# Performance work log

Hardware: AMD Instinct MI355X
Metric: run time of the kernel (lower is better)

The kernel has to match this reference:

```python
import jax, jax.numpy as jnp
import numpy as np

B, S, D = 8, 2048, 768
SCALE = jnp.sqrt(jnp.float32(D))


def setup_inputs() -> dict:
    key = jax.random.key(0)
    ks = jax.random.split(key, 9)
    sd = 1.0 / np.sqrt(D)
    return {
        "x": jax.random.normal(ks[0], (B, S, D), jnp.float32),
        "Wq": jax.random.normal(ks[1], (D, D), jnp.float32) * sd,
        "bq": jax.random.normal(ks[2], (D,), jnp.float32) * sd,
        "Wk": jax.random.normal(ks[3], (D, D), jnp.float32) * sd,
        "bk": jax.random.normal(ks[4], (D,), jnp.float32) * sd,
        "Wv": jax.random.normal(ks[5], (D, D), jnp.float32) * sd,
        "bv": jax.random.normal(ks[6], (D,), jnp.float32) * sd,
        "Wp": jax.random.normal(ks[7], (D, D), jnp.float32) * sd,
        "bp": jax.random.normal(ks[8], (D,), jnp.float32) * sd,
    }


def reference(x, Wq, bq, Wk, bk, Wv, bv, Wp, bp):
    # Linear layers: y = x @ W^T + b (torch nn.Linear convention)
    Q = jnp.einsum("bsd,ed->bse", x, Wq) + bq
    K = jnp.einsum("bsd,ed->bse", x, Wk) + bk
    V = jnp.einsum("bsd,ed->bse", x, Wv) + bv
    # Full attention matrix (no head split in original module)
    alpha = jnp.einsum("bqd,bkd->bqk", Q, K) / SCALE  # [B,S,S]
    alpha = jax.nn.softmax(alpha, axis=-1)
    # dropout is identity in eval mode
    out = jnp.einsum("bqk,bkd->bqd", alpha, V)
    out = jnp.einsum("bsd,ed->bse", out, Wp) + bp
    return out
```

## Files before the change

kernel.cpp:

```cpp
#include <hip/hip_runtime.h>
#include <stdint.h>


typedef __attribute__((ext_vector_type(8))) short short8;
typedef __attribute__((ext_vector_type(4))) float f32x4;

typedef const __attribute__((address_space(1))) void gvoid_t;
typedef __attribute__((address_space(3))) void lvoid_t;

__device__ __forceinline__ float b2f(unsigned short u) {
  union { unsigned int u; float f; } v;
  v.u = ((unsigned int)u) << 16;
  return v.f;
}
__device__ __forceinline__ unsigned short f2b(float f) {
  union { float f; unsigned int u; } v; v.f = f;
  unsigned int u = v.u;
  return (unsigned short)((u + 0x7fffu + ((u >> 16) & 1u)) >> 16);
}

struct Cvt9 {
  const void* s[9];
  unsigned short* d[9];
  long long n8[9];
  long long total8;
};

__global__ __launch_bounds__(256) void convert_inputs(Cvt9 C) {
  long long g = (long long)blockIdx.x * 256 + threadIdx.x;
  if (g >= C.total8) return;
  int s = 0;
  long long off = g;
  while (off >= C.n8[s]) { off -= C.n8[s]; ++s; }
  const float* sf = (const float*)C.s[s] + off * 8;
  unsigned short* dp = C.d[s] + off * 8;
  float4 a = ((const float4*)sf)[0];
  float4 b = ((const float4*)sf)[1];
  uint4 o;
  o.x = (unsigned int)f2b(a.x) | ((unsigned int)f2b(a.y) << 16);
  o.y = (unsigned int)f2b(a.z) | ((unsigned int)f2b(a.w) << 16);
  o.z = (unsigned int)f2b(b.x) | ((unsigned int)f2b(b.y) << 16);
  o.w = (unsigned int)f2b(b.z) | ((unsigned int)f2b(b.w) << 16);
  *(uint4*)dp = o;
}

__device__ __forceinline__ void gemm256(
    const unsigned short* __restrict__ Ag,
    const unsigned short* __restrict__ Bg,
    const int lda, const int ldb, const int NT,
    unsigned short* lds, f32x4 (&acc)[4][4])
{
  const int t    = threadIdx.x;
  const int w    = t >> 6;
  const int lane = t & 63;
  const int lo   = lane & 15;
  const int quad = lane >> 4;
  const int wr   = w >> 1;
  const int wc   = w & 1;
  const int srow = t >> 2;
  const int ssw  = ((t & 3) ^ ((t >> 3) & 3)) << 3;

  const unsigned lbase = (unsigned)(uintptr_t)(void*)lds;
  const unsigned rsw   = (unsigned)((quad ^ ((lo >> 1) & 3)) << 4);
  const unsigned aAr   = lbase + (unsigned)(wr * 64 + lo) * 64 + rsw;
  const unsigned aBr   = lbase + 16384u + (unsigned)(wc * 64 + lo) * 64 + rsw;

#define STG(kt, buf) {                                                              \
  const unsigned short* a0_ = Ag + (size_t)(srow)       * lda + (kt) * 32 + ssw;    \
  const unsigned short* a1_ = Ag + (size_t)(128 + srow) * lda + (kt) * 32 + ssw;    \
  const unsigned short* b0_ = Bg + (size_t)(srow)       * ldb + (kt) * 32 + ssw;    \
  unsigned short* d_ = lds + (buf) * 12288 + t * 8;                                 \
  __builtin_amdgcn_global_load_lds((gvoid_t*)a0_, (lvoid_t*)(d_),        16, 0, 0); \
  __builtin_amdgcn_global_load_lds((gvoid_t*)a1_, (lvoid_t*)(d_ + 4096), 16, 0, 0); \
  __builtin_amdgcn_global_load_lds((gvoid_t*)b0_, (lvoid_t*)(d_ + 8192), 16, 0, 0); }
#define DSR(d, a, IMM) asm volatile("ds_read_b128 %0, %1 offset:" #IMM : "=v"(d) : "v"(a))
#define LGK(n) { asm volatile("s_waitcnt lgkmcnt(" #n ")" ::: "memory"); \
                 __builtin_amdgcn_sched_barrier(0); }
#define GRP(g) { _Pragma("unroll") for (int mi = 0; mi < 4; ++mi)             \
    acc[mi][g] = __builtin_amdgcn_mfma_f32_16x16x32_bf16(                     \
        af[mi], bf[g], acc[mi][g], 0, 0, 0); }

  STG(0, 0);
  __syncthreads();

  for (int kt = 0; kt < NT; ++kt) {
    const int buf = kt & 1;
    if (kt + 1 < NT) STG(kt + 1, buf ^ 1);

    const unsigned bo = (unsigned)(buf * 24576);
    short8 af[4], bf[4];
    const unsigned aA = aAr + bo, aB = aBr + bo;
    DSR(af[0], aA, 0); DSR(af[1], aA, 1024); DSR(af[2], aA, 2048); DSR(af[3], aA, 3072);
    DSR(bf[0], aB, 0); DSR(bf[1], aB, 1024); DSR(bf[2], aB, 2048); DSR(bf[3], aB, 3072);

    __builtin_amdgcn_s_setprio(1);
    LGK(3); GRP(0);
    LGK(2); GRP(1);
    LGK(1); GRP(2);
    LGK(0); GRP(3);
    __builtin_amdgcn_s_setprio(0);

    __syncthreads();
  }
#undef STG
#undef DSR
#undef LGK
#undef GRP
}

template<int MODE>
__device__ __forceinline__ void epi_bf16(
    unsigned short* Ls, f32x4 (&acc)[4][4],
    const unsigned short* bias_n0, const float* rlbase, float scale,
    unsigned short* Cg, int ldc, float* rlout)
{
  const int t = threadIdx.x, w = t >> 6, lane = t & 63;
  const int lo = lane & 15, quad = lane >> 4, wr = w >> 1, wc = w & 1;
#pragma unroll
  for (int h = 0; h < 2; ++h) {
    __syncthreads();
    if ((wr >> 1) == h) {
      float bvv[4];
      if (MODE == 0) {
#pragma unroll
        for (int ni = 0; ni < 4; ++ni) bvv[ni] = b2f(bias_n0[wc * 64 + ni * 16 + lo]);
      }
#pragma unroll
      for (int mi = 0; mi < 4; ++mi) {
        const int r0 = (wr & 1) * 64 + mi * 16 + quad * 4;
        float rv[4];
        if (MODE == 3) {
#pragma unroll
          for (int r = 0; r < 4; ++r) rv[r] = __builtin_amdgcn_rcpf(rlbase[h * 128 + r0 + r]);
        }
#pragma unroll
        for (int ni = 0; ni < 4; ++ni) {
          const int col = wc * 64 + ni * 16 + lo;
#pragma unroll
          for (int r = 0; r < 4; ++r) {
            float v = acc[mi][ni][r];
            if (MODE == 0)      v += bvv[ni];
            else if (MODE == 2) v = __expf(fminf(v * scale, 30.f));
            else if (MODE == 3) v *= rv[r];
            Ls[(r0 + r) * 136 + col] = f2b(v);
          }
        }
      }
    }
    __syncthreads();
#pragma unroll
    for (int j = 0; j < 4; ++j) {
      const int u = j * 512 + t, row = u >> 4, c16 = (u & 15) * 8;
      *(uint4*)(Cg + (size_t)(h * 128 + row) * ldc + c16) = *(const uint4*)(Ls + row * 136 + c16);
    }
    if (MODE == 2) {
      const int row = t >> 2, seg = t & 3;
      const unsigned short* lr = Ls + row * 136 + seg * 32;
      float s = 0.f;
#pragma unroll
      for (int q4 = 0; q4 < 4; ++q4) {
        uint4 v = *(const uint4*)(lr + q4 * 8);
        unsigned int uu[4] = {v.x, v.y, v.z, v.w};
#pragma unroll
        for (int c = 0; c < 4; ++c)
          s += b2f((unsigned short)(uu[c] & 0xffffu)) + b2f((unsigned short)(uu[c] >> 16));
      }
      s += __shfl_xor(s, 1);
      s += __shfl_xor(s, 2);
      if (seg == 0) atomicAdd(rlout + h * 128 + row, s);
    }
  }
}

__global__ __launch_bounds__(512, 4) void qkv_k(
    const unsigned short* __restrict__ xb,
    const unsigned short* __restrict__ Wq, const unsigned short* __restrict__ bq,
    const unsigned short* __restrict__ Wk, const unsigned short* __restrict__ bk,
    const unsigned short* __restrict__ Wv, const unsigned short* __restrict__ bv,
    unsigned short* __restrict__ qb, unsigned short* __restrict__ kb,
    unsigned short* __restrict__ vt)
{
  __shared__ unsigned short smem[24576];
  const int sel = blockIdx.y / 6;
  const int n0  = (blockIdx.y % 6) * 128;
  const int m0  = blockIdx.x * 256;

  const unsigned short* W;
  const unsigned short* bi;
  if (sel == 0)      { W = Wq; bi = bq; }
  else if (sel == 1) { W = Wk; bi = bk; }
  else               { W = Wv; bi = bv; }

  f32x4 acc[4][4] = {};
  gemm256(xb + (size_t)m0 * 768, W + (size_t)n0 * 768, 768, 768, 24, smem, acc);

  if (sel < 2) {
    unsigned short* dst = (sel == 0 ? qb : kb) + (size_t)m0 * 768 + n0;
    epi_bf16<0>(smem, acc, bi + n0, nullptr, 0.f, dst, 768, nullptr);
    return;
  }

  const int t = threadIdx.x, w = t >> 6, lane = t & 63;
  const int lo = lane & 15, quad = lane >> 4, wr = w >> 1, wc = w & 1;
  const int bb2 = m0 >> 11, sin = m0 & 2047;
  unsigned short* Ls = smem;
#pragma unroll
  for (int ec = 0; ec < 2; ++ec) {
    __syncthreads();
    if (wc == ec) {
#pragma unroll
      for (int ni = 0; ni < 4; ++ni) {
        const int el = ni * 16 + lo;
        const float bvv = b2f(bi[n0 + ec * 64 + el]);
#pragma unroll
        for (int mi = 0; mi < 4; ++mi) {
          const int sl = wr * 64 + mi * 16 + quad * 4;
          ushort4 pk;
          pk.x = f2b(acc[mi][ni][0] + bvv);
          pk.y = f2b(acc[mi][ni][1] + bvv);
          pk.z = f2b(acc[mi][ni][2] + bvv);
          pk.w = f2b(acc[mi][ni][3] + bvv);
          *(ushort4*)(Ls + el * 264 + sl) = pk;
        }
      }
    }
    __syncthreads();
    unsigned short* Vb = vt + (size_t)bb2 * 1572864 + (size_t)(n0 + ec * 64) * 2048 + sin;
#pragma unroll
    for (int j = 0; j < 4; ++j) {
      const int u = j * 512 + t, e = u >> 5, s16 = (u & 31) * 8;
      *(uint4*)(Vb + (size_t)e * 2048 + s16) = *(const uint4*)(Ls + e * 264 + s16);
    }
  }
}

__global__ __launch_bounds__(512, 4) void score_k(
    const unsigned short* __restrict__ Q, const unsigned short* __restrict__ Kb,
    unsigned short* __restrict__ E, float* __restrict__ rl, float scale)
{
  __shared__ unsigned short smem[24576];
  const int m0 = blockIdx.x * 256, n0 = blockIdx.y * 128, bz = blockIdx.z;

  f32x4 acc[4][4] = {};
  gemm256(Q + (size_t)bz * 1572864 + (size_t)m0 * 768,
          Kb + (size_t)bz * 1572864 + (size_t)n0 * 768, 768, 768, 24, smem, acc);

  unsigned short* Eg = E + (size_t)bz * 4194304 + (size_t)m0 * 2048 + n0;
  epi_bf16<2>(smem, acc, nullptr, nullptr, scale, Eg, 2048, rl + bz * 2048 + m0);
}

__global__ __launch_bounds__(512, 4) void pv_k(
    const unsigned short* __restrict__ E, const unsigned short* __restrict__ Vt,
    const float* __restrict__ rl, unsigned short* __restrict__ attn)
{
  __shared__ unsigned short smem[24576];
  const int m0 = blockIdx.x * 256, n0 = blockIdx.y * 128, bz = blockIdx.z;

  f32x4 acc[4][4] = {};
  gemm256(E + (size_t)bz * 4194304 + (size_t)m0 * 2048,
          Vt + (size_t)bz * 1572864 + (size_t)n0 * 2048, 2048, 2048, 64, smem, acc);

  const float* rlb = rl + bz * 2048 + m0;
  unsigned short* Cg = attn + (size_t)bz * 1572864 + (size_t)m0 * 768 + n0;
  epi_bf16<3>(smem, acc, nullptr, rlb, 0.f, Cg, 768, nullptr);
}

__global__ __launch_bounds__(512, 4) void out_k(
    const unsigned short* __restrict__ attn,
    const unsigned short* __restrict__ Wp, const unsigned short* __restrict__ bp,
    float* __restrict__ Of)
{
  __shared__ unsigned short smem[24576];
  const int m0 = blockIdx.x * 256, n0 = blockIdx.y * 128;

  f32x4 acc[4][4] = {};
  gemm256(attn + (size_t)m0 * 768, Wp + (size_t)n0 * 768, 768, 768, 24, smem, acc);

  const int t = threadIdx.x, w = t >> 6, lane = t & 63;
  const int lo = lane & 15, quad = lane >> 4, wr = w >> 1, wc = w & 1;
  float* Lf = (float*)smem;
#pragma unroll
  for (int p = 0; p < 4; ++p) {
    __syncthreads();
    if (wr == p) {
#pragma unroll
      for (int mi = 0; mi < 4; ++mi) {
        const int r0 = mi * 16 + quad * 4;
#pragma unroll
        for (int ni = 0; ni < 4; ++ni) {
          const int col = wc * 64 + ni * 16 + lo;
          const float bvv = b2f(bp[n0 + col]);
#pragma unroll
          for (int r = 0; r < 4; ++r)
            Lf[(r0 + r) * 132 + col] = acc[mi][ni][r] + bvv;
        }
      }
    }
    __syncthreads();
#pragma unroll
    for (int j = 0; j < 2; ++j) {
      const int u = j * 512 + t, row = u >> 4, c4 = (u & 15) * 8;
      const float* src = Lf + row * 132 + c4;
      float4 v0 = *(const float4*)(src);
      float4 v1 = *(const float4*)(src + 4);
      float* dst = Of + (size_t)(m0 + p * 64 + row) * 768 + n0 + c4;
      *(float4*)(dst) = v0;
      *(float4*)(dst + 4) = v1;
    }
  }
}

extern "C" void kernel_launch(void* const* d_in, const int* in_sizes, int n_in,
                              void* d_out, int out_size, void* d_ws, size_t ws_size,
                              hipStream_t stream) {
  (void)in_sizes; (void)n_in; (void)out_size; (void)ws_size;

  char* ws = (char*)d_ws;
  float* rl    = (float*)(ws + 4096);
  unsigned short* wcv = (unsigned short*)(ws + ((size_t)1 << 20));
  unsigned short* qb  = (unsigned short*)(ws + ((size_t)8  << 20));
  unsigned short* kb  = (unsigned short*)(ws + ((size_t)32 << 20));
  unsigned short* vt  = (unsigned short*)(ws + ((size_t)56 << 20));
  unsigned short* eb  = (unsigned short*)(ws + ((size_t)80 << 20));
  unsigned short* xb  = eb;
  unsigned short* attn = qb;

  unsigned short* wqb = wcv;
  unsigned short* bqb = wcv + 589824;
  unsigned short* wkb = wcv + 590592;
  unsigned short* bkb = wcv + 1180416;
  unsigned short* wvb = wcv + 1181184;
  unsigned short* bvb = wcv + 1771008;
  unsigned short* wpb = wcv + 1771776;
  unsigned short* bpb = wcv + 2361600;

  const float inv_scale = 0.036084391824351615f;

  Cvt9 cv;
  cv.s[0] = d_in[0]; cv.d[0] = xb;  cv.n8[0] = 12582912 / 8;
  cv.s[1] = d_in[1]; cv.d[1] = wqb; cv.n8[1] = 589824 / 8;
  cv.s[2] = d_in[2]; cv.d[2] = bqb; cv.n8[2] = 768 / 8;
  cv.s[3] = d_in[3]; cv.d[3] = wkb; cv.n8[3] = 589824 / 8;
  cv.s[4] = d_in[4]; cv.d[4] = bkb; cv.n8[4] = 768 / 8;
  cv.s[5] = d_in[5]; cv.d[5] = wvb; cv.n8[5] = 589824 / 8;
  cv.s[6] = d_in[6]; cv.d[6] = bvb; cv.n8[6] = 768 / 8;
  cv.s[7] = d_in[7]; cv.d[7] = wpb; cv.n8[7] = 589824 / 8;
  cv.s[8] = d_in[8]; cv.d[8] = bpb; cv.n8[8] = 768 / 8;
  cv.total8 = (12582912 + 4 * (589824 + 768)) / 8;
  convert_inputs<<<(unsigned)((cv.total8 + 255) / 256), dim3(256), 0, stream>>>(cv);

  hipMemsetAsync(rl, 0, 16384 * sizeof(float), stream);

  qkv_k<<<dim3(64, 18, 1), dim3(512), 0, stream>>>(xb, wqb, bqb, wkb, bkb, wvb, bvb, qb, kb, vt);

  score_k<<<dim3(8, 16, 8), dim3(512), 0, stream>>>(qb, kb, eb, rl, inv_scale);

  pv_k<<<dim3(8, 6, 8), dim3(512), 0, stream>>>(eb, vt, rl, attn);

  out_k<<<dim3(64, 6, 1), dim3(512), 0, stream>>>(attn, wpb, bpb, (float*)d_out);
}
```

Measured before the change: 342.2 us.

## Halve block size and double per-wave M tile in all GEMM kernels

Each GEMM block now runs 4 waves (256 threads) instead of 8. Every wave computes a 128x64 output tile with 8x4 MFMA accumulators, where before it was 64x64. Staging issues six global-to-LDS loads per thread instead of three, and the epilogues are reindexed to match. The goal is more MFMA work per LDS fragment read and fewer waves per block. The cost is doubled accumulator registers, which could cut occupancy or cause spills, and less parallelism for hiding latency.

```diff
diff --git a/kernel.cpp b/kernel.cpp
--- a/kernel.cpp
+++ b/kernel.cpp
@@ -48,11 +48,11 @@
     const unsigned short* __restrict__ Ag,
     const unsigned short* __restrict__ Bg,
     const int lda, const int ldb, const int NT,
-    unsigned short* lds, f32x4 (&acc)[4][4])
+    unsigned short* lds, f32x4 (&acc)[8][4])
 {
   const int t    = threadIdx.x;
+  const int lane = t & 63;
   const int w    = t >> 6;
-  const int lane = t & 63;
   const int lo   = lane & 15;
   const int quad = lane >> 4;
   const int wr   = w >> 1;
@@ -62,21 +62,27 @@
 
   const unsigned lbase = (unsigned)(uintptr_t)(void*)lds;
   const unsigned rsw   = (unsigned)((quad ^ ((lo >> 1) & 3)) << 4);
-  const unsigned aAr   = lbase + (unsigned)(wr * 64 + lo) * 64 + rsw;
+  const unsigned aAr   = lbase + (unsigned)(wr * 128 + lo) * 64 + rsw;
   const unsigned aBr   = lbase + 16384u + (unsigned)(wc * 64 + lo) * 64 + rsw;
 
 #define STG(kt, buf) {                                                              \
   const unsigned short* a0_ = Ag + (size_t)(srow)       * lda + (kt) * 32 + ssw;    \
-  const unsigned short* a1_ = Ag + (size_t)(128 + srow) * lda + (kt) * 32 + ssw;    \
+  const unsigned short* a1_ = Ag + (size_t)(64 + srow)  * lda + (kt) * 32 + ssw;    \
+  const unsigned short* a2_ = Ag + (size_t)(128 + srow) * lda + (kt) * 32 + ssw;    \
+  const unsigned short* a3_ = Ag + (size_t)(192 + srow) * lda + (kt) * 32 + ssw;    \
   const unsigned short* b0_ = Bg + (size_t)(srow)       * ldb + (kt) * 32 + ssw;    \
+  const unsigned short* b1_ = Bg + (size_t)(64 + srow)  * ldb + (kt) * 32 + ssw;    \
   unsigned short* d_ = lds + (buf) * 12288 + t * 8;                                 \
-  __builtin_amdgcn_global_load_lds((gvoid_t*)a0_, (lvoid_t*)(d_),        16, 0, 0); \
-  __builtin_amdgcn_global_load_lds((gvoid_t*)a1_, (lvoid_t*)(d_ + 4096), 16, 0, 0); \
-  __builtin_amdgcn_global_load_lds((gvoid_t*)b0_, (lvoid_t*)(d_ + 8192), 16, 0, 0); }
+  __builtin_amdgcn_global_load_lds((gvoid_t*)a0_, (lvoid_t*)(d_),         16, 0, 0);\
+  __builtin_amdgcn_global_load_lds((gvoid_t*)a1_, (lvoid_t*)(d_ + 2048),  16, 0, 0);\
+  __builtin_amdgcn_global_load_lds((gvoid_t*)a2_, (lvoid_t*)(d_ + 4096),  16, 0, 0);\
+  __builtin_amdgcn_global_load_lds((gvoid_t*)a3_, (lvoid_t*)(d_ + 6144),  16, 0, 0);\
+  __builtin_amdgcn_global_load_lds((gvoid_t*)b0_, (lvoid_t*)(d_ + 8192),  16, 0, 0);\
+  __builtin_amdgcn_global_load_lds((gvoid_t*)b1_, (lvoid_t*)(d_ + 10240), 16, 0, 0); }
 #define DSR(d, a, IMM) asm volatile("ds_read_b128 %0, %1 offset:" #IMM : "=v"(d) : "v"(a))
 #define LGK(n) { asm volatile("s_waitcnt lgkmcnt(" #n ")" ::: "memory"); \
                  __builtin_amdgcn_sched_barrier(0); }
-#define GRP(g) { _Pragma("unroll") for (int mi = 0; mi < 4; ++mi)             \
+#define GRP(g) { _Pragma("unroll") for (int mi = 0; mi < 8; ++mi)             \
     acc[mi][g] = __builtin_amdgcn_mfma_f32_16x16x32_bf16(                     \
         af[mi], bf[g], acc[mi][g], 0, 0, 0); }
 
@@ -88,10 +94,14 @@
     if (kt + 1 < NT) STG(kt + 1, buf ^ 1);
 
     const unsigned bo = (unsigned)(buf * 24576);
-    short8 af[4], bf[4];
+    short8 af[8], bf[4];
     const unsigned aA = aAr + bo, aB = aBr + bo;
-    DSR(af[0], aA, 0); DSR(af[1], aA, 1024); DSR(af[2], aA, 2048); DSR(af[3], aA, 3072);
-    DSR(bf[0], aB, 0); DSR(bf[1], aB, 1024); DSR(bf[2], aB, 2048); DSR(bf[3], aB, 3072);
+    DSR(af[0], aA, 0);    DSR(af[1], aA, 1024);
+    DSR(af[2], aA, 2048); DSR(af[3], aA, 3072);
+    DSR(af[4], aA, 4096); DSR(af[5], aA, 5120);
+    DSR(af[6], aA, 6144); DSR(af[7], aA, 7168);
+    DSR(bf[0], aB, 0);    DSR(bf[1], aB, 1024);
+    DSR(bf[2], aB, 2048); DSR(bf[3], aB, 3072);
 
     __builtin_amdgcn_s_setprio(1);
     LGK(3); GRP(0);
@@ -110,7 +120,7 @@
 
 template<int MODE>
 __device__ __forceinline__ void epi_bf16(
-    unsigned short* Ls, f32x4 (&acc)[4][4],
+    unsigned short* Ls, f32x4 (&acc)[8][4],
     const unsigned short* bias_n0, const float* rlbase, float scale,
     unsigned short* Cg, int ldc, float* rlout)
 {
@@ -119,15 +129,15 @@
 #pragma unroll
   for (int h = 0; h < 2; ++h) {
     __syncthreads();
-    if ((wr >> 1) == h) {
+    if (wr == h) {
       float bvv[4];
       if (MODE == 0) {
 #pragma unroll
         for (int ni = 0; ni < 4; ++ni) bvv[ni] = b2f(bias_n0[wc * 64 + ni * 16 + lo]);
       }
 #pragma unroll
-      for (int mi = 0; mi < 4; ++mi) {
-        const int r0 = (wr & 1) * 64 + mi * 16 + quad * 4;
+      for (int mi = 0; mi < 8; ++mi) {
+        const int r0 = mi * 16 + quad * 4;
         float rv[4];
         if (MODE == 3) {
 #pragma unroll
@@ -149,30 +159,29 @@
     }
     __syncthreads();
 #pragma unroll
-    for (int j = 0; j < 4; ++j) {
-      const int u = j * 512 + t, row = u >> 4, c16 = (u & 15) * 8;
+    for (int j = 0; j < 8; ++j) {
+      const int u = j * 256 + t, row = u >> 4, c16 = (u & 15) * 8;
       *(uint4*)(Cg + (size_t)(h * 128 + row) * ldc + c16) = *(const uint4*)(Ls + row * 136 + c16);
     }
     if (MODE == 2) {
-      const int row = t >> 2, seg = t & 3;
-      const unsigned short* lr = Ls + row * 136 + seg * 32;
+      const int row = t >> 1, seg = t & 1;
+      const unsigned short* lr = Ls + row * 136 + seg * 64;
       float s = 0.f;
 #pragma unroll
-      for (int q4 = 0; q4 < 4; ++q4) {
-        uint4 v = *(const uint4*)(lr + q4 * 8);
+      for (int q8 = 0; q8 < 8; ++q8) {
+        uint4 v = *(const uint4*)(lr + q8 * 8);
         unsigned int uu[4] = {v.x, v.y, v.z, v.w};
 #pragma unroll
         for (int c = 0; c < 4; ++c)
           s += b2f((unsigned short)(uu[c] & 0xffffu)) + b2f((unsigned short)(uu[c] >> 16));
       }
       s += __shfl_xor(s, 1);
-      s += __shfl_xor(s, 2);
       if (seg == 0) atomicAdd(rlout + h * 128 + row, s);
     }
   }
 }
 
-__global__ __launch_bounds__(512, 4) void qkv_k(
+__global__ __launch_bounds__(256, 2) void qkv_k(
     const unsigned short* __restrict__ xb,
     const unsigned short* __restrict__ Wq, const unsigned short* __restrict__ bq,
     const unsigned short* __restrict__ Wk, const unsigned short* __restrict__ bk,
@@ -191,7 +200,7 @@
   else if (sel == 1) { W = Wk; bi = bk; }
   else               { W = Wv; bi = bv; }
 
-  f32x4 acc[4][4] = {};
+  f32x4 acc[8][4] = {};
   gemm256(xb + (size_t)m0 * 768, W + (size_t)n0 * 768, 768, 768, 24, smem, acc);
 
   if (sel < 2) {
@@ -213,8 +222,8 @@
         const int el = ni * 16 + lo;
         const float bvv = b2f(bi[n0 + ec * 64 + el]);
 #pragma unroll
-        for (int mi = 0; mi < 4; ++mi) {
-          const int sl = wr * 64 + mi * 16 + quad * 4;
+        for (int mi = 0; mi < 8; ++mi) {
+          const int sl = wr * 128 + mi * 16 + quad * 4;
           ushort4 pk;
           pk.x = f2b(acc[mi][ni][0] + bvv);
           pk.y = f2b(acc[mi][ni][1] + bvv);
@@ -227,21 +236,21 @@
     __syncthreads();
     unsigned short* Vb = vt + (size_t)bb2 * 1572864 + (size_t)(n0 + ec * 64) * 2048 + sin;
 #pragma unroll
-    for (int j = 0; j < 4; ++j) {
-      const int u = j * 512 + t, e = u >> 5, s16 = (u & 31) * 8;
+    for (int j = 0; j < 8; ++j) {
+      const int u = j * 256 + t, e = u >> 5, s16 = (u & 31) * 8;
       *(uint4*)(Vb + (size_t)e * 2048 + s16) = *(const uint4*)(Ls + e * 264 + s16);
     }
   }
 }
 
-__global__ __launch_bounds__(512, 4) void score_k(
+__global__ __launch_bounds__(256, 2) void score_k(
     const unsigned short* __restrict__ Q, const unsigned short* __restrict__ Kb,
     unsigned short* __restrict__ E, float* __restrict__ rl, float scale)
 {
   __shared__ unsigned short smem[24576];
   const int m0 = blockIdx.x * 256, n0 = blockIdx.y * 128, bz = blockIdx.z;
 
-  f32x4 acc[4][4] = {};
+  f32x4 acc[8][4] = {};
   gemm256(Q + (size_t)bz * 1572864 + (size_t)m0 * 768,
           Kb + (size_t)bz * 1572864 + (size_t)n0 * 768, 768, 768, 24, smem, acc);
 
@@ -249,14 +258,14 @@
   epi_bf16<2>(smem, acc, nullptr, nullptr, scale, Eg, 2048, rl + bz * 2048 + m0);
 }
 
-__global__ __launch_bounds__(512, 4) void pv_k(
+__global__ __launch_bounds__(256, 2) void pv_k(
     const unsigned short* __restrict__ E, const unsigned short* __restrict__ Vt,
     const float* __restrict__ rl, unsigned short* __restrict__ attn)
 {
   __shared__ unsigned short smem[24576];
   const int m0 = blockIdx.x * 256, n0 = blockIdx.y * 128, bz = blockIdx.z;
 
-  f32x4 acc[4][4] = {};
+  f32x4 acc[8][4] = {};
   gemm256(E + (size_t)bz * 4194304 + (size_t)m0 * 2048,
           Vt + (size_t)bz * 1572864 + (size_t)n0 * 2048, 2048, 2048, 64, smem, acc);
 
@@ -265,7 +274,7 @@
   epi_bf16<3>(smem, acc, nullptr, rlb, 0.f, Cg, 768, nullptr);
 }
 
-__global__ __launch_bounds__(512, 4) void out_k(
+__global__ __launch_bounds__(256, 2) void out_k(
     const unsigned short* __restrict__ attn,
     const unsigned short* __restrict__ Wp, const unsigned short* __restrict__ bp,
     float* __restrict__ Of)
@@ -273,7 +282,7 @@
   __shared__ unsigned short smem[24576];
   const int m0 = blockIdx.x * 256, n0 = blockIdx.y * 128;
 
-  f32x4 acc[4][4] = {};
+  f32x4 acc[8][4] = {};
   gemm256(attn + (size_t)m0 * 768, Wp + (size_t)n0 * 768, 768, 768, 24, smem, acc);
 
   const int t = threadIdx.x, w = t >> 6, lane = t & 63;
@@ -282,30 +291,27 @@
 #pragma unroll
   for (int p = 0; p < 4; ++p) {
     __syncthreads();
-    if (wr == p) {
-#pragma unroll
-      for (int mi = 0; mi < 4; ++mi) {
-        const int r0 = mi * 16 + quad * 4;
+    if (wr == (p >> 1)) {
+#pragma unroll
+      for (int mm = 0; mm < 4; ++mm) {
+        const int mi = (p & 1) * 4 + mm;
+        const int lr0 = mm * 16 + quad * 4;
 #pragma unroll
         for (int ni = 0; ni < 4; ++ni) {
           const int col = wc * 64 + ni * 16 + lo;
           const float bvv = b2f(bp[n0 + col]);
 #pragma unroll
           for (int r = 0; r < 4; ++r)
-            Lf[(r0 + r) * 132 + col] = acc[mi][ni][r] + bvv;
+            Lf[(lr0 + r) * 132 + col] = acc[mi][ni][r] + bvv;
         }
       }
     }
     __syncthreads();
 #pragma unroll
-    for (int j = 0; j < 2; ++j) {
-      const int u = j * 512 + t, row = u >> 4, c4 = (u & 15) * 8;
-      const float* src = Lf + row * 132 + c4;
-      float4 v0 = *(const float4*)(src);
-      float4 v1 = *(const float4*)(src + 4);
-      float* dst = Of + (size_t)(m0 + p * 64 + row) * 768 + n0 + c4;
-      *(float4*)(dst) = v0;
-      *(float4*)(dst + 4) = v1;
+    for (int j = 0; j < 8; ++j) {
+      const int u = j * 256 + t, row = u >> 5, c4 = (u & 31) * 4;
+      *(float4*)(Of + (size_t)(m0 + p * 64 + row) * 768 + n0 + c4) =
+          *(const float4*)(Lf + row * 132 + c4);
     }
   }
 }
@@ -351,11 +357,11 @@
 
   hipMemsetAsync(rl, 0, 16384 * sizeof(float), stream);
 
-  qkv_k<<<dim3(64, 18, 1), dim3(512), 0, stream>>>(xb, wqb, bqb, wkb, bkb, wvb, bvb, qb, kb, vt);
-
-  score_k<<<dim3(8, 16, 8), dim3(512), 0, stream>>>(qb, kb, eb, rl, inv_scale);
-
-  pv_k<<<dim3(8, 6, 8), dim3(512), 0, stream>>>(eb, vt, rl, attn);
-
-  out_k<<<dim3(64, 6, 1), dim3(512), 0, stream>>>(attn, wpb, bpb, (float*)d_out);
-}
+  qkv_k<<<dim3(64, 18, 1), dim3(256), 0, stream>>>(xb, wqb, bqb, wkb, bkb, wvb, bvb, qb, kb, vt);
+
+  score_k<<<dim3(8, 16, 8), dim3(256), 0, stream>>>(qb, kb, eb, rl, inv_scale);
+
+  pv_k<<<dim3(8, 6, 8), dim3(256), 0, stream>>>(eb, vt, rl, attn);
+
+  out_k<<<dim3(64, 6, 1), dim3(256), 0, stream>>>(attn, wpb, bpb, (float*)d_out);
+}
```

Result: slower. 356.3 us (+4.1%).
